# Kernel tuning notes

Hardware: AMD Instinct MI355X
Metric: run time of the kernel (lower is better)

Reference implementation:

```python
import jax, jax.numpy as jnp
import numpy as np

BS, HS, IN_DIM, OUT_DIM = 256, 512, 64, 4


def setup_inputs() -> dict:
    key = jax.random.key(0)
    ks = jax.random.split(key, 14)
    u = lambda k, shp, s: s * jax.random.uniform(k, shp, dtype=jnp.float32)
    n = lambda k, shp: jax.random.normal(k, shp, dtype=jnp.float32)
    # Linear layers: PyTorch default init ~ U(-1/sqrt(fan_in), 1/sqrt(fan_in)); plain uniform is fine for a reference.
    bi_s = 1.0 / np.sqrt(IN_DIM)
    bh_s = 1.0 / np.sqrt(HS)
    return {
        "inputs": n(ks[0], (BS, IN_DIM)),
        "hidden": n(ks[1], (BS, HS)),
        "hebb": n(ks[2], (BS, HS, HS)),
        "Wi": u(ks[3], (HS, IN_DIM), bi_s),   # i2h weight
        "bi": u(ks[4], (HS,), bi_s),
        "w": 0.01 * jax.random.uniform(ks[5], (HS, HS), dtype=jnp.float32),      # fixed recurrent weights
        "alpha": 0.01 * jax.random.uniform(ks[6], (HS, HS), dtype=jnp.float32),  # plasticity coefficients
        "Wo": u(ks[7], (OUT_DIM, HS), bh_s),  # h2o
        "bo": u(ks[8], (OUT_DIM,), bh_s),
        "Wv": u(ks[9], (1, HS), bh_s),        # h2v
        "bv": u(ks[10], (1,), bh_s),
        "Wda": u(ks[11], (1, HS), bh_s),      # h2DA
        "bda": u(ks[12], (1,), bh_s),
    }


def reference(inputs, hidden, hebb, Wi, bi, w, alpha, Wo, bo, Wv, bv, Wda, bda):
    # hactiv = tanh(i2h(x) + (w + alpha*hebb) @ hidden)
    rec = hidden @ w.T + jnp.einsum("ij,bij,bj->bi", alpha, hebb, hidden)  # [B,HS]
    hactiv = jnp.tanh(inputs @ Wi.T + bi + rec)                              # [B,HS]
    activout = hactiv @ Wo.T + bo                                            # [B,OUT]
    valueout = hactiv @ Wv.T + bv                                            # [B,1]
    DAout = jnp.tanh(hactiv @ Wda.T + bda)                                   # [B,1] (da='tanh')
    # deltahebb = outer(hactiv, hidden); fm=1 -> fully DA-modulated update
    deltahebb = hactiv[:, :, None] * hidden[:, None, :]                      # [B,HS,HS]
    hebb_new = jnp.clip(hebb + DAout[:, :, None] * deltahebb, -1.0, 1.0)
    return activout, valueout, DAout, hactiv, hebb_new
```

## Files before the change

### kernel.cpp

```cpp
#include <hip/hip_runtime.h>

#define BS 256
#define HS 512
#define IN_DIM 64
#define OUT_DIM 4

typedef float nfloat4 __attribute__((ext_vector_type(4)));

__global__ __launch_bounds__(256) void rec_kernel(
    const float* __restrict__ hidden,
    const float* __restrict__ hebb,
    const float* __restrict__ w,
    const float* __restrict__ alpha,
    float* __restrict__ rec)
{
    const int row  = blockIdx.x * 4 + (threadIdx.x >> 6);
    const int lane = threadIdx.x & 63;
    const int b = row >> 9;
    const int i = row & (HS - 1);

    const float4* __restrict__ hebb4 = (const float4*)(hebb + (size_t)row * HS);
    const float4* __restrict__ w4    = (const float4*)(w     + (size_t)i * HS);
    const float4* __restrict__ a4    = (const float4*)(alpha + (size_t)i * HS);
    const float4* __restrict__ h4    = (const float4*)(hidden + (size_t)b * HS);

    float sum = 0.f;
#pragma unroll
    for (int t = 0; t < 2; ++t) {
        const int idx = lane + t * 64;
        const float4 hb = hebb4[idx];
        const float4 ww = w4[idx];
        const float4 aa = a4[idx];
        const float4 hh = h4[idx];
        sum += hh.x * (ww.x + aa.x * hb.x);
        sum += hh.y * (ww.y + aa.y * hb.y);
        sum += hh.z * (ww.z + aa.z * hb.z);
        sum += hh.w * (ww.w + aa.w * hb.w);
    }
#pragma unroll
    for (int off = 32; off > 0; off >>= 1)
        sum += __shfl_xor(sum, off, 64);
    if (lane == 0) rec[row] = sum;
}

__global__ __launch_bounds__(512) void act_kernel(
    const float* __restrict__ inputs,
    const float* __restrict__ Wi, const float* __restrict__ bi,
    const float* __restrict__ rec,
    const float* __restrict__ Wo, const float* __restrict__ bo,
    const float* __restrict__ Wv, const float* __restrict__ bv,
    const float* __restrict__ Wda, const float* __restrict__ bda,
    float* __restrict__ activout, float* __restrict__ valueout,
    float* __restrict__ daout, float* __restrict__ hactiv,
    float* __restrict__ scale)
{
    const int b = blockIdx.x;
    const int i = threadIdx.x;

    __shared__ __align__(16) float sh_in[IN_DIM];
    __shared__ float red[8][8];
    __shared__ float da_sh;

    if (i < IN_DIM) sh_in[i] = inputs[b * IN_DIM + i];
    __syncthreads();

    float dot = 0.f;
    const float4* __restrict__ wi4 = (const float4*)(Wi + (size_t)i * IN_DIM);
    const float4* __restrict__ in4 = (const float4*)sh_in;
#pragma unroll
    for (int t = 0; t < IN_DIM / 4; ++t) {
        const float4 a = wi4[t];
        const float4 x = in4[t];
        dot += a.x * x.x + a.y * x.y + a.z * x.z + a.w * x.w;
    }

    const float h = tanhf(dot + bi[i] + rec[(size_t)b * HS + i]);
    hactiv[(size_t)b * HS + i] = h;

    float p[6];
    p[0] = h * Wo[0 * HS + i];
    p[1] = h * Wo[1 * HS + i];
    p[2] = h * Wo[2 * HS + i];
    p[3] = h * Wo[3 * HS + i];
    p[4] = h * Wv[i];
    p[5] = h * Wda[i];

    const int lane = i & 63, wave = i >> 6;
#pragma unroll
    for (int k = 0; k < 6; ++k) {
        float s = p[k];
#pragma unroll
        for (int off = 32; off > 0; off >>= 1)
            s += __shfl_xor(s, off, 64);
        if (lane == 0) red[wave][k] = s;
    }
    __syncthreads();

    if (i < 6) {
        float s = 0.f;
#pragma unroll
        for (int wv = 0; wv < 8; ++wv) s += red[wv][i];
        if (i < 4) {
            activout[b * OUT_DIM + i] = s + bo[i];
        } else if (i == 4) {
            valueout[b] = s + bv[0];
        } else {
            const float da = tanhf(s + bda[0]);
            daout[b] = da;
            da_sh = da;
        }
    }
    __syncthreads();

    scale[(size_t)b * HS + i] = da_sh * h;
}

__global__ __launch_bounds__(256) void hebb_kernel(
    const float* __restrict__ hebb,
    const float* __restrict__ hidden,
    const float* __restrict__ scale,
    float* __restrict__ hebb_new)
{
    const long long total4 = (long long)BS * HS * HS / 4;
    const long long stride = (long long)gridDim.x * blockDim.x;
    const long long tid    = (long long)blockIdx.x * blockDim.x + threadIdx.x;
    for (long long v = total4 - 1 - tid; v >= 0; v -= stride) {
        const long long e = v * 4;
        const int b = (int)(e >> 18);
        const int i = (int)(e >> 9) & (HS - 1);
        const int j = (int)e & (HS - 1);

        const float s = scale[b * HS + i];
        const float4 hid = *(const float4*)(hidden + b * HS + j);
        const float4 hb  = ((const float4*)hebb)[v];
        nfloat4 o;
        o.x = fminf(fmaxf(hb.x + s * hid.x, -1.f), 1.f);
        o.y = fminf(fmaxf(hb.y + s * hid.y, -1.f), 1.f);
        o.z = fminf(fmaxf(hb.z + s * hid.z, -1.f), 1.f);
        o.w = fminf(fmaxf(hb.w + s * hid.w, -1.f), 1.f);
        __builtin_nontemporal_store(o, (nfloat4*)hebb_new + v);
    }
}

extern "C" void kernel_launch(void* const* d_in, const int* in_sizes, int n_in,
                              void* d_out, int out_size, void* d_ws, size_t ws_size,
                              hipStream_t stream) {
    const float* inputs = (const float*)d_in[0];
    const float* hidden = (const float*)d_in[1];
    const float* hebb   = (const float*)d_in[2];
    const float* Wi     = (const float*)d_in[3];
    const float* bi     = (const float*)d_in[4];
    const float* w      = (const float*)d_in[5];
    const float* alpha  = (const float*)d_in[6];
    const float* Wo     = (const float*)d_in[7];
    const float* bo     = (const float*)d_in[8];
    const float* Wv     = (const float*)d_in[9];
    const float* bv     = (const float*)d_in[10];
    const float* Wda    = (const float*)d_in[11];
    const float* bda    = (const float*)d_in[12];

    float* out = (float*)d_out;
    float* activout = out;
    float* valueout = out + 1024;
    float* daout    = out + 1280;
    float* hactiv   = out + 1536;
    float* hebb_new = out + 1536 + BS * HS;

    float* rec   = (float*)d_ws;
    float* scale = rec;

    rec_kernel<<<(BS * HS) / 4, 256, 0, stream>>>(hidden, hebb, w, alpha, rec);

    act_kernel<<<BS, HS, 0, stream>>>(inputs, Wi, bi, rec, Wo, bo, Wv, bv,
                                      Wda, bda, activout, valueout, daout,
                                      hactiv, scale);

    hebb_kernel<<<2048, 256, 0, stream>>>(hebb, hidden, scale, hebb_new);
}
```

Measured before the change: 138.5 us.

## Fuse rec, activation and hebb update into one per-batch kernel

Replaces the three kernels with a single kernel launched with one 1024-thread block per batch row. Each block computes the plastic recurrent term, the activation and heads, and then the hebb update, keeping intermediates in shared memory. The intent is to drop the launch gaps and workspace round trips, and to have the second hebb read hit cache because the block has just read that slice. The cost is only one block per CU and serialized phases within each block, which may limit memory-level parallelism.

```diff
diff --git a/kernel.cpp b/kernel.cpp
--- a/kernel.cpp
+++ b/kernel.cpp
@@ -7,85 +7,83 @@
 
 typedef float nfloat4 __attribute__((ext_vector_type(4)));
 
-__global__ __launch_bounds__(256) void rec_kernel(
+__global__ __launch_bounds__(1024) void fused_kernel(
+    const float* __restrict__ inputs,
     const float* __restrict__ hidden,
     const float* __restrict__ hebb,
-    const float* __restrict__ w,
-    const float* __restrict__ alpha,
-    float* __restrict__ rec)
-{
-    const int row  = blockIdx.x * 4 + (threadIdx.x >> 6);
-    const int lane = threadIdx.x & 63;
-    const int b = row >> 9;
-    const int i = row & (HS - 1);
-
-    const float4* __restrict__ hebb4 = (const float4*)(hebb + (size_t)row * HS);
-    const float4* __restrict__ w4    = (const float4*)(w     + (size_t)i * HS);
-    const float4* __restrict__ a4    = (const float4*)(alpha + (size_t)i * HS);
-    const float4* __restrict__ h4    = (const float4*)(hidden + (size_t)b * HS);
-
-    float sum = 0.f;
-#pragma unroll
-    for (int t = 0; t < 2; ++t) {
-        const int idx = lane + t * 64;
-        const float4 hb = hebb4[idx];
-        const float4 ww = w4[idx];
-        const float4 aa = a4[idx];
-        const float4 hh = h4[idx];
-        sum += hh.x * (ww.x + aa.x * hb.x);
-        sum += hh.y * (ww.y + aa.y * hb.y);
-        sum += hh.z * (ww.z + aa.z * hb.z);
-        sum += hh.w * (ww.w + aa.w * hb.w);
-    }
-#pragma unroll
-    for (int off = 32; off > 0; off >>= 1)
-        sum += __shfl_xor(sum, off, 64);
-    if (lane == 0) rec[row] = sum;
-}
-
-__global__ __launch_bounds__(512) void act_kernel(
-    const float* __restrict__ inputs,
-    const float* __restrict__ Wi, const float* __restrict__ bi,
-    const float* __restrict__ rec,
-    const float* __restrict__ Wo, const float* __restrict__ bo,
-    const float* __restrict__ Wv, const float* __restrict__ bv,
+    const float* __restrict__ Wi,  const float* __restrict__ bi,
+    const float* __restrict__ w,   const float* __restrict__ alpha,
+    const float* __restrict__ Wo,  const float* __restrict__ bo,
+    const float* __restrict__ Wv,  const float* __restrict__ bv,
     const float* __restrict__ Wda, const float* __restrict__ bda,
     float* __restrict__ activout, float* __restrict__ valueout,
-    float* __restrict__ daout, float* __restrict__ hactiv,
-    float* __restrict__ scale)
+    float* __restrict__ daout,    float* __restrict__ hactiv,
+    float* __restrict__ hebb_new)
 {
-    const int b = blockIdx.x;
-    const int i = threadIdx.x;
+    const int b    = blockIdx.x;
+    const int tid  = threadIdx.x;
+    const int wave = tid >> 6;
+    const int lane = tid & 63;
 
+    __shared__ __align__(16) float sh_hidden[HS];
     __shared__ __align__(16) float sh_in[IN_DIM];
-    __shared__ float red[8][8];
+    __shared__ float sh_rec[HS];
+    __shared__ float sh_scale[HS];
+    __shared__ float red[16][6];
     __shared__ float da_sh;
 
-    if (i < IN_DIM) sh_in[i] = inputs[b * IN_DIM + i];
+    if (tid < HS / 4)
+        ((float4*)sh_hidden)[tid] = ((const float4*)(hidden + (size_t)b * HS))[tid];
+    if (tid >= 512 && tid < 512 + IN_DIM / 4)
+        ((float4*)sh_in)[tid - 512] = ((const float4*)(inputs + (size_t)b * IN_DIM))[tid - 512];
     __syncthreads();
 
-    float dot = 0.f;
-    const float4* __restrict__ wi4 = (const float4*)(Wi + (size_t)i * IN_DIM);
-    const float4* __restrict__ in4 = (const float4*)sh_in;
+    const float4* __restrict__ hebb4b = (const float4*)(hebb + (size_t)b * HS * HS);
+    for (int r = 0; r < 32; ++r) {
+        const int i = wave * 32 + r;
+        const float4* __restrict__ h4 = hebb4b + i * (HS / 4);
+        const float4* __restrict__ w4 = (const float4*)(w     + (size_t)i * HS);
+        const float4* __restrict__ a4 = (const float4*)(alpha + (size_t)i * HS);
+        float sum = 0.f;
 #pragma unroll
-    for (int t = 0; t < IN_DIM / 4; ++t) {
-        const float4 a = wi4[t];
-        const float4 x = in4[t];
-        dot += a.x * x.x + a.y * x.y + a.z * x.z + a.w * x.w;
+        for (int t = 0; t < 2; ++t) {
+            const int idx = lane + t * 64;
+            const float4 hb = h4[idx];
+            const float4 ww = w4[idx];
+            const float4 aa = a4[idx];
+            const float4 hh = ((const float4*)sh_hidden)[idx];
+            sum += hh.x * (ww.x + aa.x * hb.x);
+            sum += hh.y * (ww.y + aa.y * hb.y);
+            sum += hh.z * (ww.z + aa.z * hb.z);
+            sum += hh.w * (ww.w + aa.w * hb.w);
+        }
+#pragma unroll
+        for (int off = 32; off > 0; off >>= 1)
+            sum += __shfl_xor(sum, off, 64);
+        if (lane == 0) sh_rec[i] = sum;
     }
+    __syncthreads();
 
-    const float h = tanhf(dot + bi[i] + rec[(size_t)b * HS + i]);
-    hactiv[(size_t)b * HS + i] = h;
-
-    float p[6];
-    p[0] = h * Wo[0 * HS + i];
-    p[1] = h * Wo[1 * HS + i];
-    p[2] = h * Wo[2 * HS + i];
-    p[3] = h * Wo[3 * HS + i];
-    p[4] = h * Wv[i];
-    p[5] = h * Wda[i];
-
-    const int lane = i & 63, wave = i >> 6;
+    float h = 0.f;
+    float p[6] = {0.f, 0.f, 0.f, 0.f, 0.f, 0.f};
+    if (tid < HS) {
+        float dot = 0.f;
+        const float4* __restrict__ wi4 = (const float4*)(Wi + (size_t)tid * IN_DIM);
+#pragma unroll
+        for (int t = 0; t < IN_DIM / 4; ++t) {
+            const float4 a = wi4[t];
+            const float4 x = ((const float4*)sh_in)[t];
+            dot += a.x * x.x + a.y * x.y + a.z * x.z + a.w * x.w;
+        }
+        h = tanhf(dot + bi[tid] + sh_rec[tid]);
+        hactiv[(size_t)b * HS + tid] = h;
+        p[0] = h * Wo[0 * HS + tid];
+        p[1] = h * Wo[1 * HS + tid];
+        p[2] = h * Wo[2 * HS + tid];
+        p[3] = h * Wo[3 * HS + tid];
+        p[4] = h * Wv[tid];
+        p[5] = h * Wda[tid];
+    }
 #pragma unroll
     for (int k = 0; k < 6; ++k) {
         float s = p[k];
@@ -96,13 +94,13 @@
     }
     __syncthreads();
 
-    if (i < 6) {
+    if (tid < 6) {
         float s = 0.f;
 #pragma unroll
-        for (int wv = 0; wv < 8; ++wv) s += red[wv][i];
-        if (i < 4) {
-            activout[b * OUT_DIM + i] = s + bo[i];
-        } else if (i == 4) {
+        for (int wv = 0; wv < 16; ++wv) s += red[wv][tid];
+        if (tid < 4) {
+            activout[b * OUT_DIM + tid] = s + bo[tid];
+        } else if (tid == 4) {
             valueout[b] = s + bv[0];
         } else {
             const float da = tanhf(s + bda[0]);
@@ -112,33 +110,25 @@
     }
     __syncthreads();
 
-    scale[(size_t)b * HS + i] = da_sh * h;
-}
+    if (tid < HS) sh_scale[tid] = da_sh * h;
+    __syncthreads();
 
-__global__ __launch_bounds__(256) void hebb_kernel(
-    const float* __restrict__ hebb,
-    const float* __restrict__ hidden,
-    const float* __restrict__ scale,
-    float* __restrict__ hebb_new)
-{
-    const long long total4 = (long long)BS * HS * HS / 4;
-    const long long stride = (long long)gridDim.x * blockDim.x;
-    const long long tid    = (long long)blockIdx.x * blockDim.x + threadIdx.x;
-    for (long long v = total4 - 1 - tid; v >= 0; v -= stride) {
-        const long long e = v * 4;
-        const int b = (int)(e >> 18);
-        const int i = (int)(e >> 9) & (HS - 1);
-        const int j = (int)e & (HS - 1);
-
-        const float s = scale[b * HS + i];
-        const float4 hid = *(const float4*)(hidden + b * HS + j);
-        const float4 hb  = ((const float4*)hebb)[v];
-        nfloat4 o;
-        o.x = fminf(fmaxf(hb.x + s * hid.x, -1.f), 1.f);
-        o.y = fminf(fmaxf(hb.y + s * hid.y, -1.f), 1.f);
-        o.z = fminf(fmaxf(hb.z + s * hid.z, -1.f), 1.f);
-        o.w = fminf(fmaxf(hb.w + s * hid.w, -1.f), 1.f);
-        __builtin_nontemporal_store(o, (nfloat4*)hebb_new + v);
+    nfloat4* __restrict__ dst = (nfloat4*)(hebb_new + (size_t)b * HS * HS);
+    for (int r = 0; r < 32; ++r) {
+        const int i = wave * 32 + r;
+        const float s = sh_scale[i];
+#pragma unroll
+        for (int t = 0; t < 2; ++t) {
+            const int idx = i * (HS / 4) + lane + t * 64;
+            const float4 hb = hebb4b[idx];
+            const float4 hh = ((const float4*)sh_hidden)[lane + t * 64];
+            nfloat4 o;
+            o.x = fminf(fmaxf(hb.x + s * hh.x, -1.f), 1.f);
+            o.y = fminf(fmaxf(hb.y + s * hh.y, -1.f), 1.f);
+            o.z = fminf(fmaxf(hb.z + s * hh.z, -1.f), 1.f);
+            o.w = fminf(fmaxf(hb.w + s * hh.w, -1.f), 1.f);
+            __builtin_nontemporal_store(o, dst + idx);
+        }
     }
 }
 
@@ -166,14 +156,8 @@
     float* hactiv   = out + 1536;
     float* hebb_new = out + 1536 + BS * HS;
 
-    float* rec   = (float*)d_ws;
-    float* scale = rec;
-
-    rec_kernel<<<(BS * HS) / 4, 256, 0, stream>>>(hidden, hebb, w, alpha, rec);
-
-    act_kernel<<<BS, HS, 0, stream>>>(inputs, Wi, bi, rec, Wo, bo, Wv, bv,
-                                      Wda, bda, activout, valueout, daout,
-                                      hactiv, scale);
-
-    hebb_kernel<<<2048, 256, 0, stream>>>(hebb, hidden, scale, hebb_new);
+    fused_kernel<<<BS, 1024, 0, stream>>>(inputs, hidden, hebb, Wi, bi, w, alpha,
+                                          Wo, bo, Wv, bv, Wda, bda,
+                                          activout, valueout, daout, hactiv,
+                                          hebb_new);
 }
```

Measured after the change: 145.7 us. 5.2% more time.
